# Optimization experiments

Hardware: AMD Instinct MI355X
Metric: run time of the kernel (lower is better)

Reference implementation:

```python
import jax, jax.numpy as jnp
import numpy as np

NUM_HEADS = 8

def _qkv(t, W, b, H):
    # t: [B, L, C] -> q, k, v each [B, H, L, D]
    B, L, C = t.shape
    D = C // H
    qkv = (t @ W + b).reshape(B, L, 3, H, D)
    qkv = jnp.moveaxis(qkv, 2, 0)           # [3, B, L, H, D]
    qkv = jnp.swapaxes(qkv, 2, 3)           # [3, B, H, L, D]
    return qkv[0], qkv[1], qkv[2]

def _attend(q, k, v, scale):
    # q,k,v: [B, H, L, D] -> [B, L, C]
    B, H, L, D = q.shape
    scores = jnp.einsum('bhqd,bhkd->bhqk', q, k) * scale
    attn = jax.nn.softmax(scores, axis=-1)
    out = jnp.einsum('bhqk,bhkd->bhqd', attn, v)
    return jnp.swapaxes(out, 1, 2).reshape(B, L, H * D)

def setup_inputs() -> dict:
    key = jax.random.key(0)
    ks = jax.random.split(key, 7)
    B, N, C = 8, 2048, 512
    s_in = 1.0 / np.sqrt(C)
    return {
        'x': jax.random.normal(ks[0], (B, N, C), dtype=jnp.float32),
        'W_rgb_qkv': jax.random.normal(ks[1], (C, 3 * C), dtype=jnp.float32) * s_in,
        'b_rgb_qkv': jax.random.normal(ks[2], (3 * C,), dtype=jnp.float32) * 0.02,
        'W_depth_qkv': jax.random.normal(ks[3], (C, 3 * C), dtype=jnp.float32) * s_in,
        'b_depth_qkv': jax.random.normal(ks[4], (3 * C,), dtype=jnp.float32) * 0.02,
        'W_proj': jax.random.normal(ks[5], (C, C), dtype=jnp.float32) * s_in,
        'b_proj': jax.random.normal(ks[6], (C,), dtype=jnp.float32) * 0.02,
    }

def reference(x, W_rgb_qkv, b_rgb_qkv, W_depth_qkv, b_depth_qkv, W_proj, b_proj):
    B, N, C = x.shape
    H = NUM_HEADS
    D = C // H
    scale = D ** -0.5
    L = N // 2
    rgb, depth = x[:, :L], x[:, L:]
    rq, rk, rv = _qkv(rgb, W_rgb_qkv, b_rgb_qkv, H)
    dq, dk, dv = _qkv(depth, W_depth_qkv, b_depth_qkv, H)
    # rgb queries attend to depth K/V (named depth_v in torch code)
    depth_out = _attend(rq, dk, dv, scale)
    # depth queries attend to rgb K/V (named rgb_v in torch code)
    rgb_out = _attend(dq, rk, rv, scale)
    out = jnp.concatenate([rgb_out, depth_out], axis=1)  # [B, N, C]
    return out @ W_proj + b_proj
```

## Files before the change

kernel.cpp:

```cpp
#include <hip/hip_runtime.h>
#include <hip/hip_bf16.h>

typedef __attribute__((ext_vector_type(8))) short s16x8;
typedef __attribute__((ext_vector_type(4))) float f32x4;

__device__ __forceinline__ ushort f2bf(float f) {
  union { float f; unsigned int u; } c; c.f = f;
  unsigned int u = c.u + 0x7fffu + ((c.u >> 16) & 1u);
  return (ushort)(u >> 16);
}

__device__ __forceinline__ unsigned int pack2(float lo, float hi) {
  __hip_bfloat162 b2 = __float22bfloat162_rn(make_float2(lo, hi));
  union { __hip_bfloat162 b; unsigned int u; } c; c.b = b2;
  return c.u;
}

__device__ __forceinline__ s16x8 ld16(const ushort* p) {
  union { uint4 u; s16x8 s; } c;
  c.u = *reinterpret_cast<const uint4*>(p);
  return c.s;
}

__device__ __forceinline__ f32x4 mfma16(s16x8 a, s16x8 b, f32x4 c) {
  return __builtin_amdgcn_mfma_f32_16x16x32_bf16(a, b, c, 0, 0, 0);
}

__device__ __forceinline__ float exp2fast(float x) { return __builtin_amdgcn_exp2f(x); }

__device__ __forceinline__ void gld_lds16(const void* g, void* l) {
  __builtin_amdgcn_global_load_lds(
      (const __attribute__((address_space(1))) void*)g,
      (__attribute__((address_space(3))) void*)l, 16, 0, 0);
}


__global__ __launch_bounds__(256) void k_prep(
    const float* __restrict__ x, ushort* __restrict__ xb,
    const float* __restrict__ Wr, ushort* __restrict__ WtR,
    const float* __restrict__ Wd, ushort* __restrict__ WtD,
    const float* __restrict__ Wp, ushort* __restrict__ WtP) {
  __shared__ float tile[32][33];
  int b = blockIdx.x, t = threadIdx.x;
  if (b < 8192) {
    int i = (b * 256 + t) * 4;
    float4 v = *reinterpret_cast<const float4*>(x + i);
    ushort4 o;
    o.x = f2bf(v.x); o.y = f2bf(v.y); o.z = f2bf(v.z); o.w = f2bf(v.w);
    *reinterpret_cast<ushort4*>(xb + i) = o;
    return;
  }
  b -= 8192;
  const float* src; ushort* dst; int N;
  if (b < 768)      { src = Wr; dst = WtR; N = 1536; }
  else if (b < 1536){ b -= 768;  src = Wd; dst = WtD; N = 1536; }
  else              { b -= 1536; src = Wp; dst = WtP; N = 512; }
  int nb = N >> 5;
  int n0 = (b % nb) * 32, k0 = (b / nb) * 32;
  int tx = t & 31, ty = t >> 5;
#pragma unroll
  for (int i = 0; i < 32; i += 8)
    tile[ty + i][tx] = src[(k0 + ty + i) * N + (n0 + tx)];
  __syncthreads();
#pragma unroll
  for (int i = 0; i < 32; i += 8)
    dst[(size_t)(n0 + ty + i) * 512 + (k0 + tx)] = f2bf(tile[tx][ty + i]);
}


__device__ __forceinline__ void stage_lds(const ushort* __restrict__ src, int ld,
                                          char* ldsbase, int t) {
#pragma unroll
  for (int p = 0; p < 4; ++p) {
    int chunk = p * 256 + t;
    int r = chunk >> 3, cc = chunk & 7;
    gld_lds16(src + r * ld + ((cc ^ (r & 7)) * 8), ldsbase + (chunk & ~63) * 16);
  }
}

__device__ __forceinline__ s16x8 lds_frag(const char* lds, int row, int c) {
  union { uint4 u; s16x8 s; } cv;
  cv.u = *reinterpret_cast<const uint4*>(lds + row * 128 + ((c ^ (row & 7)) * 16));
  return cv.s;
}


template <bool TRANS>
__global__ __launch_bounds__(256) void k_qkv(
    const ushort* __restrict__ xb, const ushort* __restrict__ WtR,
    const ushort* __restrict__ WtD, const float* __restrict__ bR,
    const float* __restrict__ bD, ushort* __restrict__ Qb,
    ushort* __restrict__ Kb, ushort* __restrict__ Vt) {
  __shared__ __align__(16) char lds[65536];
  int m0 = blockIdx.x * 128;
  int n0 = (TRANS ? 1024 : 0) + blockIdx.y * 128;
  int s = m0 >> 13, bb = (m0 >> 10) & 7, lbase = m0 & 1023;
  const ushort* A = xb + (size_t)(bb * 2048 + s * 1024 + lbase) * 512;
  const ushort* Wt = (s ? WtD : WtR) + (size_t)n0 * 512;
  const float* bias = s ? bD : bR;
  int t = threadIdx.x;
  int wid = t >> 6, ln = t & 15, g = (t & 63) >> 4;
  int wr = wid >> 1, wc = wid & 1;
  f32x4 acc[4][4] = {};
  stage_lds(A, 512, lds, t);
  stage_lds(Wt, 512, lds + 16384, t);
  __syncthreads();
  for (int ks = 0; ks < 8; ++ks) {
    char* cbuf = lds + (ks & 1) * 32768;
    if (ks < 7) {
      char* nbuf = lds + ((ks + 1) & 1) * 32768;
      stage_lds(A + (ks + 1) * 64, 512, nbuf, t);
      stage_lds(Wt + (ks + 1) * 64, 512, nbuf + 16384, t);
    }
    char* ldsA = cbuf;
    char* ldsB = cbuf + 16384;
#pragma unroll
    for (int kk = 0; kk < 2; ++kk) {
      s16x8 af[4], bf[4];
#pragma unroll
      for (int mi = 0; mi < 4; ++mi) af[mi] = lds_frag(ldsA, wr * 64 + mi * 16 + ln, kk * 4 + g);
#pragma unroll
      for (int ni = 0; ni < 4; ++ni) bf[ni] = lds_frag(ldsB, wc * 64 + ni * 16 + ln, kk * 4 + g);
#pragma unroll
      for (int mi = 0; mi < 4; ++mi)
#pragma unroll
        for (int ni = 0; ni < 4; ++ni)
          acc[mi][ni] = TRANS ? mfma16(bf[ni], af[mi], acc[mi][ni])
                              : mfma16(af[mi], bf[ni], acc[mi][ni]);
    }
    __syncthreads();
  }
  int hb_base = (s * 8 + bb) * 8;
  if (!TRANS) {
    bool isK = (n0 >> 9) != 0;
    ushort* dst = isK ? Kb : Qb;
    float sc = isK ? 1.0f : 0.18033688011112042f;
#pragma unroll
    for (int mi = 0; mi < 4; ++mi)
#pragma unroll
      for (int ni = 0; ni < 4; ++ni) {
        f32x4 v = acc[mi][ni];
        int col = n0 + wc * 64 + ni * 16 + ln;
        int h = (col >> 6) & 7, d = col & 63;
        float bv = bias[col];
        ushort* hp = dst + ((size_t)(hb_base + h) << 16);
        int lr = lbase + wr * 64 + mi * 16 + g * 4;
#pragma unroll
        for (int j = 0; j < 4; ++j) hp[(lr + j) * 64 + d] = f2bf((v[j] + bv) * sc);
      }
  } else {
#pragma unroll
    for (int mi = 0; mi < 4; ++mi)
#pragma unroll
      for (int ni = 0; ni < 4; ++ni) {
        f32x4 v = acc[mi][ni];
        int nb = n0 + wc * 64 + ni * 16 + g * 4;
        int mm = m0 + wr * 64 + mi * 16 + ln;
        int l = mm & 1023;
        int lp = (l & ~63) | (l & 0x23) | ((l & 0x0C) << 1) | ((l & 0x10) >> 2);
#pragma unroll
        for (int j = 0; j < 4; ++j) {
          int col = nb + j;
          int h = (col >> 6) & 7, d = col & 63;
          Vt[((size_t)(hb_base + h) << 16) + d * 1024 + lp] = f2bf(v[j] + bias[col]);
        }
      }
  }
}


__global__ __launch_bounds__(256, 5) void k_attn(const ushort* __restrict__ Qb,
                                                 const ushort* __restrict__ Kb,
                                                 const ushort* __restrict__ Vt,
                                                 ushort* __restrict__ AO) {
  __shared__ __align__(16) char lds[32768];
  int bid = blockIdx.x;
  int set = bid & 127, qb = bid >> 7;
  int pair = set & 1, h = (set >> 1) & 7, bb = set >> 4;
  int sQ = 1 - pair, sKV = pair;
  const ushort* Qp = Qb + ((size_t)((sQ * 8 + bb) * 8 + h) << 16);
  const ushort* Kp = Kb + ((size_t)((sKV * 8 + bb) * 8 + h) << 16);
  const ushort* Vp = Vt + ((size_t)((sKV * 8 + bb) * 8 + h) << 16);
  int t = threadIdx.x, w = t >> 6, l = t & 63, ln = t & 15, g = (t & 63) >> 4;
  int q0 = qb * 128 + w * 32;
  s16x8 qf0a = ld16(Qp + (q0 + ln) * 64 + g * 8);
  s16x8 qf1a = ld16(Qp + (q0 + ln) * 64 + 32 + g * 8);
  s16x8 qf0b = ld16(Qp + (q0 + 16 + ln) * 64 + g * 8);
  s16x8 qf1b = ld16(Qp + (q0 + 16 + ln) * 64 + 32 + g * 8);

  int cA = w * 128 + l;
  int cB = w * 128 + 64 + l;
  int rA = cA >> 3, ccA = cA & 7;
  int rB = cB >> 3, ccB = cB & 7;
  int kofA = rA * 64 + ((ccA ^ (rA & 7)) * 8);
  int kofB = rB * 64 + ((ccB ^ (rB & 7)) * 8);
  int vofA = rA * 1024 + ((ccA ^ (rA & 7)) * 8);
  int vofB = rB * 1024 + ((ccB ^ (rB & 7)) * 8);

  float ls_a = 0.f, ls_b = 0.f;
  f32x4 oca[4] = {}, ocb[4] = {};

  {
    char* base = lds;
    gld_lds16(Kp + kofA, base + w * 2048);
    gld_lds16(Kp + kofB, base + w * 2048 + 1024);
    gld_lds16(Vp + vofA, base + 8192 + w * 2048);
    gld_lds16(Vp + vofB, base + 8192 + w * 2048 + 1024);
  }
  __syncthreads();

  int cur = 0;
  for (int it = 0; it < 16; ++it) {
    int t0 = it * 64;
    if (it < 15) {
      char* base = lds + (cur ^ 1) * 16384;
      const ushort* kp = Kp + (t0 + 64) * 64;
      const ushort* vp = Vp + (t0 + 64);
      gld_lds16(kp + kofA, base + w * 2048);
      gld_lds16(kp + kofB, base + w * 2048 + 1024);
      gld_lds16(vp + vofA, base + 8192 + w * 2048);
      gld_lds16(vp + vofB, base + 8192 + w * 2048 + 1024);
    }
    const char* ldsK = lds + cur * 16384;
    const char* ldsV = ldsK + 8192;

    f32x4 za[4], zb[4];
#pragma unroll
    for (int s = 0; s < 4; ++s) {
      s16x8 k0 = lds_frag(ldsK, s * 16 + ln, g);
      s16x8 k1 = lds_frag(ldsK, s * 16 + ln, 4 + g);
      f32x4 z1 = {}; z1 = mfma16(k0, qf0a, z1); z1 = mfma16(k1, qf1a, z1); za[s] = z1;
      f32x4 z2 = {}; z2 = mfma16(k0, qf0b, z2); z2 = mfma16(k1, qf1b, z2); zb[s] = z2;
    }

    unsigned int pwa[8], pwb[8];
#pragma unroll
    for (int s = 0; s < 4; ++s) {
      float p0 = exp2fast(za[s][0]), p1 = exp2fast(za[s][1]);
      float p2 = exp2fast(za[s][2]), p3 = exp2fast(za[s][3]);
      ls_a += (p0 + p1) + (p2 + p3);
      pwa[2 * s] = pack2(p0, p1); pwa[2 * s + 1] = pack2(p2, p3);
      float r0 = exp2fast(zb[s][0]), r1 = exp2fast(zb[s][1]);
      float r2 = exp2fast(zb[s][2]), r3 = exp2fast(zb[s][3]);
      ls_b += (r0 + r1) + (r2 + r3);
      pwb[2 * s] = pack2(r0, r1); pwb[2 * s + 1] = pack2(r2, r3);
    }
    union { uint4 u; s16x8 v; } c0, c1, c2, c3;
    c0.u = make_uint4(pwa[0], pwa[1], pwa[2], pwa[3]);
    c1.u = make_uint4(pwa[4], pwa[5], pwa[6], pwa[7]);
    c2.u = make_uint4(pwb[0], pwb[1], pwb[2], pwb[3]);
    c3.u = make_uint4(pwb[4], pwb[5], pwb[6], pwb[7]);
    s16x8 pf0a = c0.v, pf1a = c1.v, pf0b = c2.v, pf1b = c3.v;

#pragma unroll
    for (int d = 0; d < 4; ++d) {
      s16x8 v0 = lds_frag(ldsV, d * 16 + ln, g);
      s16x8 v1 = lds_frag(ldsV, d * 16 + ln, 4 + g);
      oca[d] = mfma16(v0, pf0a, oca[d]);
      oca[d] = mfma16(v1, pf1a, oca[d]);
      ocb[d] = mfma16(v0, pf0b, ocb[d]);
      ocb[d] = mfma16(v1, pf1b, ocb[d]);
    }
    __syncthreads();
    cur ^= 1;
  }

  ls_a += __shfl_xor(ls_a, 16, 64);
  ls_a += __shfl_xor(ls_a, 32, 64);
  ls_b += __shfl_xor(ls_b, 16, 64);
  ls_b += __shfl_xor(ls_b, 32, 64);
  float inva = 1.0f / ls_a, invb = 1.0f / ls_b;
  int orow = bb * 2048 + pair * 1024 + q0 + ln;
#pragma unroll
  for (int d = 0; d < 4; ++d) {
    uint2 st;
    st.x = pack2(oca[d][0] * inva, oca[d][1] * inva);
    st.y = pack2(oca[d][2] * inva, oca[d][3] * inva);
    *reinterpret_cast<uint2*>(AO + (size_t)orow * 512 + h * 64 + d * 16 + 4 * g) = st;
    uint2 st2;
    st2.x = pack2(ocb[d][0] * invb, ocb[d][1] * invb);
    st2.y = pack2(ocb[d][2] * invb, ocb[d][3] * invb);
    *reinterpret_cast<uint2*>(AO + (size_t)(orow + 16) * 512 + h * 64 + d * 16 + 4 * g) = st2;
  }
}


__global__ __launch_bounds__(256) void k_gemm_proj(const ushort* __restrict__ AO,
                                                   const ushort* __restrict__ WtP,
                                                   const float* __restrict__ bP,
                                                   float* __restrict__ Out) {
  __shared__ __align__(16) char lds[65536];
  int m0 = blockIdx.x * 128, n0 = blockIdx.y * 128;
  const ushort* A = AO + (size_t)m0 * 512;
  const ushort* Wt = WtP + (size_t)n0 * 512;
  int t = threadIdx.x;
  int wid = t >> 6, ln = t & 15, g = (t & 63) >> 4;
  int wr = wid >> 1, wc = wid & 1;
  f32x4 acc[4][4] = {};
  stage_lds(A, 512, lds, t);
  stage_lds(Wt, 512, lds + 16384, t);
  __syncthreads();
  for (int ks = 0; ks < 8; ++ks) {
    char* cbuf = lds + (ks & 1) * 32768;
    if (ks < 7) {
      char* nbuf = lds + ((ks + 1) & 1) * 32768;
      stage_lds(A + (ks + 1) * 64, 512, nbuf, t);
      stage_lds(Wt + (ks + 1) * 64, 512, nbuf + 16384, t);
    }
    char* ldsA = cbuf;
    char* ldsB = cbuf + 16384;
#pragma unroll
    for (int kk = 0; kk < 2; ++kk) {
      s16x8 af[4], bf[4];
#pragma unroll
      for (int mi = 0; mi < 4; ++mi) af[mi] = lds_frag(ldsA, wr * 64 + mi * 16 + ln, kk * 4 + g);
#pragma unroll
      for (int ni = 0; ni < 4; ++ni) bf[ni] = lds_frag(ldsB, wc * 64 + ni * 16 + ln, kk * 4 + g);
#pragma unroll
      for (int mi = 0; mi < 4; ++mi)
#pragma unroll
        for (int ni = 0; ni < 4; ++ni) acc[mi][ni] = mfma16(af[mi], bf[ni], acc[mi][ni]);
    }
    __syncthreads();
  }
#pragma unroll
  for (int mi = 0; mi < 4; ++mi)
#pragma unroll
    for (int ni = 0; ni < 4; ++ni) {
      f32x4 v = acc[mi][ni];
      int col = n0 + wc * 64 + ni * 16 + ln;
      float bv = bP[col];
      int r0 = m0 + wr * 64 + mi * 16 + g * 4;
#pragma unroll
      for (int j = 0; j < 4; ++j) Out[(size_t)(r0 + j) * 512 + col] = v[j] + bv;
    }
}


extern "C" void kernel_launch(void* const* d_in, const int* in_sizes, int n_in,
                              void* d_out, int out_size, void* d_ws, size_t ws_size,
                              hipStream_t stream) {
  const float* x      = (const float*)d_in[0];
  const float* W_rgb  = (const float*)d_in[1];
  const float* b_rgb  = (const float*)d_in[2];
  const float* W_dep  = (const float*)d_in[3];
  const float* b_dep  = (const float*)d_in[4];
  const float* W_proj = (const float*)d_in[5];
  const float* b_proj = (const float*)d_in[6];
  float* out = (float*)d_out;

  char* ws = (char*)d_ws;
  ushort* xb  = (ushort*)(ws + 0);
  ushort* WtR = (ushort*)(ws + 16777216);
  ushort* WtD = (ushort*)(ws + 18350080);
  ushort* WtP = (ushort*)(ws + 19922944);
  ushort* Qb  = (ushort*)(ws + 20447232);
  ushort* Kb  = (ushort*)(ws + 37224448);
  ushort* Vt  = (ushort*)(ws + 54001664);
  ushort* AO  = (ushort*)(ws + 70778880);

  k_prep<<<9984, 256, 0, stream>>>(x, xb, W_rgb, WtR, W_dep, WtD, W_proj, WtP);
  k_qkv<false><<<dim3(128, 8), 256, 0, stream>>>(xb, WtR, WtD, b_rgb, b_dep, Qb, Kb, Vt);
  k_qkv<true><<<dim3(128, 4), 256, 0, stream>>>(xb, WtR, WtD, b_rgb, b_dep, Qb, Kb, Vt);
  k_attn<<<1024, 256, 0, stream>>>(Qb, Kb, Vt, AO);
  k_gemm_proj<<<dim3(128, 4), 256, 0, stream>>>(AO, WtP, b_proj, out);
}
```

Baseline: 161.1 us.

## Triple-buffer K/V tiles in attention with explicit vmcnt waits

The attention kernel's K/V staging moves from double to triple buffering in LDS (48KB), prefetching two tiles ahead. The full __syncthreads is replaced by a partial s_waitcnt vmcnt(4) plus a raw s_barrier, so one tile's loads can stay in flight across the barrier. The loop is fully unrolled and the occupancy hint of 5 in launch_bounds is dropped. The larger LDS footprint cuts the number of blocks resident per CU, and the hand-written waitcnt counts must match the number of loads issued per stage.

```diff
diff --git a/kernel.cpp b/kernel.cpp
--- a/kernel.cpp
+++ b/kernel.cpp
@@ -169,11 +169,11 @@
 }
 
 
-__global__ __launch_bounds__(256, 5) void k_attn(const ushort* __restrict__ Qb,
-                                                 const ushort* __restrict__ Kb,
-                                                 const ushort* __restrict__ Vt,
-                                                 ushort* __restrict__ AO) {
-  __shared__ __align__(16) char lds[32768];
+__global__ __launch_bounds__(256) void k_attn(const ushort* __restrict__ Qb,
+                                              const ushort* __restrict__ Kb,
+                                              const ushort* __restrict__ Vt,
+                                              ushort* __restrict__ AO) {
+  __shared__ __align__(16) char lds[49152];
   int bid = blockIdx.x;
   int set = bid & 127, qb = bid >> 7;
   int pair = set & 1, h = (set >> 1) & 7, bb = set >> 4;
@@ -200,28 +200,26 @@
   float ls_a = 0.f, ls_b = 0.f;
   f32x4 oca[4] = {}, ocb[4] = {};
 
-  {
-    char* base = lds;
-    gld_lds16(Kp + kofA, base + w * 2048);
-    gld_lds16(Kp + kofB, base + w * 2048 + 1024);
-    gld_lds16(Vp + vofA, base + 8192 + w * 2048);
-    gld_lds16(Vp + vofB, base + 8192 + w * 2048 + 1024);
-  }
-  __syncthreads();
-
-  int cur = 0;
+  auto stage = [&](int tt, char* base) {
+    const ushort* kp = Kp + tt * 4096;
+    const ushort* vp = Vp + tt * 64;
+    gld_lds16(kp + kofA, base + w * 2048);
+    gld_lds16(kp + kofB, base + w * 2048 + 1024);
+    gld_lds16(vp + vofA, base + 8192 + w * 2048);
+    gld_lds16(vp + vofB, base + 8192 + w * 2048 + 1024);
+  };
+
+  stage(0, lds);
+  stage(1, lds + 16384);
+  asm volatile("s_waitcnt vmcnt(4)" ::: "memory");
+  __builtin_amdgcn_sched_barrier(0);
+  __builtin_amdgcn_s_barrier();
+  __builtin_amdgcn_sched_barrier(0);
+
+#pragma unroll
   for (int it = 0; it < 16; ++it) {
-    int t0 = it * 64;
-    if (it < 15) {
-      char* base = lds + (cur ^ 1) * 16384;
-      const ushort* kp = Kp + (t0 + 64) * 64;
-      const ushort* vp = Vp + (t0 + 64);
-      gld_lds16(kp + kofA, base + w * 2048);
-      gld_lds16(kp + kofB, base + w * 2048 + 1024);
-      gld_lds16(vp + vofA, base + 8192 + w * 2048);
-      gld_lds16(vp + vofB, base + 8192 + w * 2048 + 1024);
-    }
-    const char* ldsK = lds + cur * 16384;
+    if (it < 14) stage(it + 2, lds + ((it + 2) % 3) * 16384);
+    const char* ldsK = lds + (it % 3) * 16384;
     const char* ldsV = ldsK + 8192;
 
     f32x4 za[4], zb[4];
@@ -261,8 +259,17 @@
       ocb[d] = mfma16(v0, pf0b, ocb[d]);
       ocb[d] = mfma16(v1, pf1b, ocb[d]);
     }
-    __syncthreads();
-    cur ^= 1;
+
+    if (it < 15) {
+      if (it < 14) {
+        asm volatile("s_waitcnt vmcnt(4)" ::: "memory");
+      } else {
+        asm volatile("s_waitcnt vmcnt(0)" ::: "memory");
+      }
+      __builtin_amdgcn_sched_barrier(0);
+      __builtin_amdgcn_s_barrier();
+      __builtin_amdgcn_sched_barrier(0);
+    }
   }
 
   ls_a += __shfl_xor(ls_a, 16, 64);
```

Result: slower. 207.1 us (+28.6%).
